# Performance work log

Hardware: AMD Instinct MI355X
Metric: run time of the kernel (lower is better)

The kernel has to match this reference:

```python
import jax, jax.numpy as jnp
import numpy as np

OBJ = 6
N_OBJS = 16
ACT = 32
HID = 128


def _mlp(x, W1, b1, W2, b2, W3, b3):
    # RoboticsMLP with layer_sizes=[128,128]: Linear->ReLU->Linear->ReLU->Linear
    h = jax.nn.relu(x @ W1 + b1)
    h = jax.nn.relu(h @ W2 + b2)
    return h @ W3 + b3


def setup_inputs() -> dict:
    key = jax.random.key(0)
    ks = jax.random.split(key, 16)
    B = 4096
    s = lambda fan_in: 1.0 / np.sqrt(fan_in)
    u_in = OBJ + ACT          # 38
    b_in = 2 * OBJ + ACT      # 44
    return {
        "config": jax.random.normal(ks[0], (B, N_OBJS * OBJ), dtype=jnp.float32),
        "action": jax.random.normal(ks[1], (B, ACT), dtype=jnp.float32),
        "uW1": jax.random.normal(ks[2], (u_in, HID), dtype=jnp.float32) * s(u_in),
        "ub1": jnp.zeros((HID,), jnp.float32),
        "uW2": jax.random.normal(ks[3], (HID, HID), dtype=jnp.float32) * s(HID),
        "ub2": jnp.zeros((HID,), jnp.float32),
        "uW3": jax.random.normal(ks[4], (HID, OBJ), dtype=jnp.float32) * s(HID),
        "ub3": jnp.zeros((OBJ,), jnp.float32),
        "bW1": jax.random.normal(ks[5], (b_in, HID), dtype=jnp.float32) * s(b_in),
        "bb1": jnp.zeros((HID,), jnp.float32),
        "bW2": jax.random.normal(ks[6], (HID, HID), dtype=jnp.float32) * s(HID),
        "bb2": jnp.zeros((HID,), jnp.float32),
        "bW3": jax.random.normal(ks[7], (HID, OBJ), dtype=jnp.float32) * s(HID),
        "bb3": jnp.zeros((OBJ,), jnp.float32),
    }


def reference(config, action, uW1, ub1, uW2, ub2, uW3, ub3,
              bW1, bb1, bW2, bb2, bW3, bb3):
    B = config.shape[0]
    objs = config.reshape(B, N_OBJS, OBJ)                       # [B, N, 6]

    # Unary: per-object MLP on [obj, action]
    act_b = jnp.broadcast_to(action[:, None, :], (B, N_OBJS, ACT))
    u_in = jnp.concatenate([objs, act_b], axis=-1)              # [B, N, 6+A]
    u_out = _mlp(u_in, uW1, ub1, uW2, ub2, uW3, ub3)            # [B, N, 6]

    # Binary: all ordered pairs (i, j), i != j: [obj_i, obj_j, action]
    oi = jnp.broadcast_to(objs[:, :, None, :], (B, N_OBJS, N_OBJS, OBJ))
    oj = jnp.broadcast_to(objs[:, None, :, :], (B, N_OBJS, N_OBJS, OBJ))
    act_p = jnp.broadcast_to(action[:, None, None, :], (B, N_OBJS, N_OBJS, ACT))
    b_in = jnp.concatenate([oi, oj, act_p], axis=-1)            # [B, N, N, 12+A]
    b_out = _mlp(b_in, bW1, bb1, bW2, bb2, bW3, bb3)            # [B, N, N, 6]

    # zero out diagonal (i == j skipped in original) then sum over j
    mask = (1.0 - jnp.eye(N_OBJS, dtype=b_out.dtype))[None, :, :, None]
    b_sum = (b_out * mask).sum(axis=2)                          # [B, N, 6]

    out = objs + u_out + b_sum
    return out.reshape(B, N_OBJS * OBJ)
```

## Files before the change

kernel.cpp:

```cpp
#include <hip/hip_runtime.h>

typedef short bf16x8 __attribute__((ext_vector_type(8)));
typedef float f32x4 __attribute__((ext_vector_type(4)));

__device__ __forceinline__ unsigned short f2bf(float f) {
    unsigned int u = __float_as_uint(f);
    unsigned int r = u + 0x7FFFu + ((u >> 16) & 1u);
    return (unsigned short)(r >> 16);
}

__device__ __forceinline__ unsigned pkbf(float a, float b) {
    unsigned r;
    asm volatile("v_cvt_pk_bf16_f32 %0, %1, %2" : "=v"(r) : "v"(a), "v"(b));
    return r;
}

__global__ __launch_bounds__(256) void prep_all(
        const float* __restrict__ uW1, const float* __restrict__ uW2, const float* __restrict__ uW3,
        const float* __restrict__ bW1, const float* __restrict__ bW2, const float* __restrict__ bW3,
        unsigned short* __restrict__ ws) {
    int idx = blockIdx.x * 256 + threadIdx.x;
    const float* W; int Ksrc, Nsrc, ntsh; unsigned short* dst; int li;
    if (idx < 8192)       { W = uW1; Ksrc = 38;  Nsrc = 128; ntsh = 10; dst = ws;         li = idx; }
    else if (idx < 16384) { W = bW1; Ksrc = 44;  Nsrc = 128; ntsh = 10; dst = ws + 8192;  li = idx - 8192; }
    else if (idx < 32768) { W = uW2; Ksrc = 128; Nsrc = 128; ntsh = 11; dst = ws + 16384; li = idx - 16384; }
    else if (idx < 49152) { W = bW2; Ksrc = 128; Nsrc = 128; ntsh = 11; dst = ws + 32768; li = idx - 32768; }
    else if (idx < 51200) { W = uW3; Ksrc = 128; Nsrc = 6;   ntsh = 11; dst = ws + 49152; li = idx - 49152; }
    else if (idx < 53248) { W = bW3; Ksrc = 128; Nsrc = 6;   ntsh = 11; dst = ws + 51200; li = idx - 51200; }
    else return;
    int e  = li & 7;
    int l  = (li >> 3) & 63;
    int KS = (ntsh == 10) ? 2 : 4;
    int ks = (li >> 9) & (KS - 1);
    int nt = li >> ntsh;
    int k  = ks * 32 + (l >> 4) * 8 + e;
    int n  = nt * 16 + (l & 15);
    float v = (k < Ksrc && n < Nsrc) ? W[k * Nsrc + n] : 0.0f;
    dst[li] = f2bf(v);
}

template <int BINARY>
__global__ __launch_bounds__(256, 3) void mlp_kernel(
        const float* __restrict__ config, const float* __restrict__ action,
        const unsigned short* __restrict__ W1f, const float* __restrict__ b1,
        const unsigned short* __restrict__ W2f, const float* __restrict__ b2,
        const unsigned short* __restrict__ W3f, const float* __restrict__ b3,
        float* __restrict__ out) {
    __shared__ __align__(16) unsigned char smem[4 * 8192];
    const int tid = threadIdx.x;
    const int w = tid >> 6;
    const int l = tid & 63;
    const int g = l >> 4;
    const int c = l & 15;
    unsigned char* buf = smem + w * 8192;

    {
        const int rowL = l >> 1;
        const int kh   = l & 1;
        const int sw   = (rowL & 7) << 4;
        const int base = rowL * 128 + kh * 64;
        const int rg = blockIdx.x * 128 + w * 32 + rowL;
        const int b = rg >> 4;
        const int i = rg & 15;
        const float* cb = config + b * 96;
        const float* ab = action + b * 32;
        if (kh == 0) {
            #pragma unroll
            for (int ch = 0; ch < 4; ++ch) {
                bf16x8 v;
                #pragma unroll
                for (int t8 = 0; t8 < 8; ++t8) {
                    const int k = ch * 8 + t8;
                    float x = (k < 6) ? cb[i * 6 + k] : ab[k - 6];
                    v[t8] = (short)f2bf(x);
                }
                *(bf16x8*)(buf + ((base + ch * 16) ^ sw)) = v;
            }
        } else {
            #pragma unroll
            for (int ch = 0; ch < 4; ++ch) {
                bf16x8 v;
                #pragma unroll
                for (int t8 = 0; t8 < 8; ++t8) {
                    const int k = 32 + ch * 8 + t8;
                    float x = (k < 38) ? ab[k - 6] : 0.0f;
                    v[t8] = (short)f2bf(x);
                }
                *(bf16x8*)(buf + ((base + ch * 16) ^ sw)) = v;
            }
        }
    }
    __syncthreads();

    const f32x4 zero4 = {0.f, 0.f, 0.f, 0.f};

    bf16x8 xf[2][2];
    #pragma unroll
    for (int mt = 0; mt < 2; ++mt)
        #pragma unroll
        for (int ks = 0; ks < 2; ++ks) {
            const int row = mt * 16 + c;
            xf[mt][ks] = *(const bf16x8*)(buf + ((row * 128 + ks * 64 + g * 16) ^ ((c & 7) << 4)));
        }

    #pragma unroll
    for (int nh = 0; nh < 2; ++nh) {
        f32x4 acc[2][4];
        #pragma unroll
        for (int mt = 0; mt < 2; ++mt)
            #pragma unroll
            for (int ntl = 0; ntl < 4; ++ntl) acc[mt][ntl] = zero4;
        #pragma unroll
        for (int ntl = 0; ntl < 4; ++ntl) {
            const int nt = nh * 4 + ntl;
            #pragma unroll
            for (int ks = 0; ks < 2; ++ks) {
                const bf16x8 bfr = *(const bf16x8*)(W1f + ((nt * 2 + ks) * 64 + l) * 8);
                #pragma unroll
                for (int mt = 0; mt < 2; ++mt)
                    acc[mt][ntl] = __builtin_amdgcn_mfma_f32_16x16x32_bf16(xf[mt][ks], bfr, acc[mt][ntl], 0, 0, 0);
            }
        }
        #pragma unroll
        for (int ntl = 0; ntl < 4; ++ntl) {
            const int col = (nh * 4 + ntl) * 16 + c;
            const float bias = b1[col];
            #pragma unroll
            for (int mt = 0; mt < 2; ++mt)
                #pragma unroll
                for (int r = 0; r < 4; ++r) {
                    const int row = mt * 16 + g * 4 + r;
                    const float hv = fmaxf(acc[mt][ntl][r] + bias, 0.f);
                    *(unsigned short*)(buf + ((row * 256 + col * 2) ^ ((row & 7) << 4))) = f2bf(hv);
                }
        }
    }
    __syncthreads();

    bf16x8 hf[2][4];
    #pragma unroll
    for (int mt = 0; mt < 2; ++mt)
        #pragma unroll
        for (int ks = 0; ks < 4; ++ks) {
            const int row = mt * 16 + c;
            hf[mt][ks] = *(const bf16x8*)(buf + ((row * 256 + ks * 64 + g * 16) ^ ((c & 7) << 4)));
        }

    #pragma unroll
    for (int nh = 0; nh < 2; ++nh) {
        f32x4 acc[2][4];
        #pragma unroll
        for (int mt = 0; mt < 2; ++mt)
            #pragma unroll
            for (int ntl = 0; ntl < 4; ++ntl) acc[mt][ntl] = zero4;
        #pragma unroll
        for (int ntl = 0; ntl < 4; ++ntl) {
            const int nt = nh * 4 + ntl;
            #pragma unroll
            for (int ks = 0; ks < 4; ++ks) {
                const bf16x8 bfr = *(const bf16x8*)(W2f + ((nt * 4 + ks) * 64 + l) * 8);
                #pragma unroll
                for (int mt = 0; mt < 2; ++mt)
                    acc[mt][ntl] = __builtin_amdgcn_mfma_f32_16x16x32_bf16(hf[mt][ks], bfr, acc[mt][ntl], 0, 0, 0);
            }
        }
        #pragma unroll
        for (int ntl = 0; ntl < 4; ++ntl) {
            const int col = (nh * 4 + ntl) * 16 + c;
            const float bias = b2[col];
            #pragma unroll
            for (int mt = 0; mt < 2; ++mt)
                #pragma unroll
                for (int r = 0; r < 4; ++r) {
                    const int row = mt * 16 + g * 4 + r;
                    const float hv = fmaxf(acc[mt][ntl][r] + bias, 0.f);
                    *(unsigned short*)(buf + ((row * 256 + col * 2) ^ ((row & 7) << 4))) = f2bf(hv);
                }
        }
    }
    __syncthreads();

    bf16x8 h2f[2][4];
    #pragma unroll
    for (int mt = 0; mt < 2; ++mt)
        #pragma unroll
        for (int ks = 0; ks < 4; ++ks) {
            const int row = mt * 16 + c;
            h2f[mt][ks] = *(const bf16x8*)(buf + ((row * 256 + ks * 64 + g * 16) ^ ((c & 7) << 4)));
        }

    f32x4 acc3[2];
    acc3[0] = zero4; acc3[1] = zero4;
    #pragma unroll
    for (int ks = 0; ks < 4; ++ks) {
        const bf16x8 bfr = *(const bf16x8*)(W3f + (ks * 64 + l) * 8);
        #pragma unroll
        for (int mt = 0; mt < 2; ++mt)
            acc3[mt] = __builtin_amdgcn_mfma_f32_16x16x32_bf16(h2f[mt][ks], bfr, acc3[mt], 0, 0, 0);
    }

    const int rgbase = blockIdx.x * 128 + w * 32;
    const float b3v = (c < 6) ? b3[c] : 0.f;
    #pragma unroll
    for (int mt = 0; mt < 2; ++mt)
        #pragma unroll
        for (int r = 0; r < 4; ++r) {
            const int rg = rgbase + mt * 16 + g * 4 + r;
            const int b = rg >> 4, i = rg & 15;
            if (c < 6) {
                const int idx = b * 96 + i * 6 + c;
                out[idx] = acc3[mt][r] + b3v + config[idx];
            }
        }
}

__global__ __launch_bounds__(256, 3) void binary_kernel(
        const float* __restrict__ config, const float* __restrict__ action,
        const unsigned short* __restrict__ W1f, const float* __restrict__ b1,
        const unsigned short* __restrict__ W2f, const float* __restrict__ b2,
        const unsigned short* __restrict__ W3f, const float* __restrict__ b3,
        float* __restrict__ out) {
    __shared__ __align__(16) unsigned char Ts[4096];
    __shared__ __align__(16) unsigned char PQs[16384];
    __shared__ __align__(16) unsigned char H2s[32768];

    const int tid = threadIdx.x;
    const int w = tid >> 6, l = tid & 63, g = l >> 4, c = l & 15;
    const int b = blockIdx.x >> 1, h = blockIdx.x & 1;
    const float* cb = config + b * 96;
    const float* ab = action + b * 32;
    const f32x4 zero4 = {0.f, 0.f, 0.f, 0.f};

    {
        const int p  = tid >> 3;
        const int k0 = (tid & 7) * 8;
        union { unsigned short us[8]; bf16x8 v; } u;
        #pragma unroll
        for (int e = 0; e < 8; ++e) {
            const int k = k0 + e;
            float x = 0.f;
            if (p < 16) {
                if (k < 6) x = cb[p * 6 + k];
                else if (k >= 12 && k < 44) x = ab[k - 12];
            } else {
                if (k >= 6 && k < 12) x = cb[(p - 16) * 6 + (k - 6)];
            }
            u.us[e] = f2bf(x);
        }
        *(bf16x8*)(Ts + ((p * 128 + k0 * 2) ^ ((p & 7) << 4))) = u.v;
    }
    __syncthreads();

    {
        bf16x8 afr[2][2];
        #pragma unroll
        for (int mt = 0; mt < 2; ++mt)
            #pragma unroll
            for (int ks = 0; ks < 2; ++ks)
                afr[mt][ks] = *(const bf16x8*)(Ts + (((c + 16 * mt) * 128 + 64 * ks + 16 * g) ^ ((c & 7) << 4)));
        f32x4 acc[2][2];
        acc[0][0] = zero4; acc[0][1] = zero4; acc[1][0] = zero4; acc[1][1] = zero4;
        #pragma unroll
        for (int ntl = 0; ntl < 2; ++ntl) {
            const int nt = 2 * w + ntl;
            #pragma unroll
            for (int ks = 0; ks < 2; ++ks) {
                const bf16x8 bfr = *(const bf16x8*)(W1f + ((nt * 2 + ks) * 64 + l) * 8);
                #pragma unroll
                for (int mt = 0; mt < 2; ++mt)
                    acc[mt][ntl] = __builtin_amdgcn_mfma_f32_16x16x32_bf16(afr[mt][ks], bfr, acc[mt][ntl], 0, 0, 0);
            }
        }
        #pragma unroll
        for (int ntl = 0; ntl < 2; ++ntl) {
            const int f = (2 * w + ntl) * 16 + c;
            const float bias = b1[f];
            #pragma unroll
            for (int mt = 0; mt < 2; ++mt)
                #pragma unroll
                for (int r = 0; r < 4; ++r) {
                    const int row = 16 * mt + 4 * g + r;
                    const float v = acc[mt][ntl][r] + (mt == 0 ? bias : 0.f);
                    *(float*)(PQs + ((row * 512 + f * 4) ^ ((row & 7) << 4))) = v;
                }
        }
    }
    __syncthreads();

    const int i0 = h * 8 + 2 * w;
    bf16x8 h1f[2][4];
    #pragma unroll
    for (int nt = 0; nt < 2; ++nt) {
        const int i = i0 + nt;
        #pragma unroll
        for (int ks = 0; ks < 4; ++ks) {
            const int kb = (32 * ks + 8 * g) * 4;
            const f32x4 p0 = *(const f32x4*)(PQs + ((i * 512 + kb) ^ ((i & 7) << 4)));
            const f32x4 p1 = *(const f32x4*)(PQs + ((i * 512 + kb + 16) ^ ((i & 7) << 4)));
            const f32x4 q0 = *(const f32x4*)(PQs + (((16 + c) * 512 + kb) ^ ((c & 7) << 4)));
            const f32x4 q1 = *(const f32x4*)(PQs + (((16 + c) * 512 + kb + 16) ^ ((c & 7) << 4)));
            union { unsigned u[4]; bf16x8 v; } un;
            un.u[0] = pkbf(fmaxf(p0[0] + q0[0], 0.f), fmaxf(p0[1] + q0[1], 0.f));
            un.u[1] = pkbf(fmaxf(p0[2] + q0[2], 0.f), fmaxf(p0[3] + q0[3], 0.f));
            un.u[2] = pkbf(fmaxf(p1[0] + q1[0], 0.f), fmaxf(p1[1] + q1[1], 0.f));
            un.u[3] = pkbf(fmaxf(p1[2] + q1[2], 0.f), fmaxf(p1[3] + q1[3], 0.f));
            h1f[nt][ks] = un.v;
        }
    }

    f32x4 acc2[8][2];
    #pragma unroll
    for (int mt = 0; mt < 8; ++mt) { acc2[mt][0] = zero4; acc2[mt][1] = zero4; }
    #pragma unroll
    for (int mt = 0; mt < 8; ++mt) {
        #pragma unroll
        for (int ks = 0; ks < 4; ++ks) {
            const bf16x8 wf = *(const bf16x8*)(W2f + ((mt * 4 + ks) * 64 + l) * 8);
            acc2[mt][0] = __builtin_amdgcn_mfma_f32_16x16x32_bf16(wf, h1f[0][ks], acc2[mt][0], 0, 0, 0);
            acc2[mt][1] = __builtin_amdgcn_mfma_f32_16x16x32_bf16(wf, h1f[1][ks], acc2[mt][1], 0, 0, 0);
        }
    }

    unsigned char* Hw = H2s + w * 8192;
    #pragma unroll
    for (int mt = 0; mt < 8; ++mt) {
        const f32x4 bv = *(const f32x4*)(b2 + 16 * mt + 4 * g);
        #pragma unroll
        for (int nt = 0; nt < 2; ++nt) {
            const int p = c + 16 * nt;
            uint2 pk2;
            pk2.x = pkbf(fmaxf(acc2[mt][nt][0] + bv[0], 0.f), fmaxf(acc2[mt][nt][1] + bv[1], 0.f));
            pk2.y = pkbf(fmaxf(acc2[mt][nt][2] + bv[2], 0.f), fmaxf(acc2[mt][nt][3] + bv[3], 0.f));
            *(uint2*)(Hw + ((p * 256 + 32 * mt + 8 * g) ^ ((c & 7) << 4))) = pk2;
        }
    }

    f32x4 acc3[2];
    acc3[0] = zero4; acc3[1] = zero4;
    #pragma unroll
    for (int ks = 0; ks < 4; ++ks) {
        const bf16x8 w3 = *(const bf16x8*)(W3f + (ks * 64 + l) * 8);
        #pragma unroll
        for (int mtA = 0; mtA < 2; ++mtA) {
            const bf16x8 hfr = *(const bf16x8*)(Hw + (((c + 16 * mtA) * 256 + 64 * ks + 16 * g) ^ ((c & 7) << 4)));
            acc3[mtA] = __builtin_amdgcn_mfma_f32_16x16x32_bf16(hfr, w3, acc3[mtA], 0, 0, 0);
        }
    }

    const float b3v = (c < 6) ? b3[c] : 0.f;
    #pragma unroll
    for (int mt = 0; mt < 2; ++mt) {
        const int i = i0 + mt;
        float s = 0.f;
        #pragma unroll
        for (int r = 0; r < 4; ++r) {
            const int j = 4 * g + r;
            if (j != i) s += acc3[mt][r] + b3v;
        }
        s += __shfl_xor(s, 16, 64);
        s += __shfl_xor(s, 32, 64);
        if (g == 0 && c < 6) out[b * 96 + i * 6 + c] += s;
    }
}

extern "C" void kernel_launch(void* const* d_in, const int* in_sizes, int n_in,
                              void* d_out, int out_size, void* d_ws, size_t ws_size,
                              hipStream_t stream) {
    const float* config = (const float*)d_in[0];
    const float* action = (const float*)d_in[1];
    const float* uW1 = (const float*)d_in[2];
    const float* ub1 = (const float*)d_in[3];
    const float* uW2 = (const float*)d_in[4];
    const float* ub2 = (const float*)d_in[5];
    const float* uW3 = (const float*)d_in[6];
    const float* ub3 = (const float*)d_in[7];
    const float* bW1 = (const float*)d_in[8];
    const float* bb1 = (const float*)d_in[9];
    const float* bW2 = (const float*)d_in[10];
    const float* bb2 = (const float*)d_in[11];
    const float* bW3 = (const float*)d_in[12];
    const float* bb3 = (const float*)d_in[13];
    float* out = (float*)d_out;

    unsigned short* ws   = (unsigned short*)d_ws;
    unsigned short* uW1f = ws;
    unsigned short* bW1f = ws + 8192;
    unsigned short* uW2f = ws + 16384;
    unsigned short* bW2f = ws + 32768;
    unsigned short* uW3f = ws + 49152;
    unsigned short* bW3f = ws + 51200;

    prep_all<<<208, 256, 0, stream>>>(uW1, uW2, uW3, bW1, bW2, bW3, ws);
    mlp_kernel<0><<<512, 256, 0, stream>>>(config, action, uW1f, ub1, uW2f, ub2, uW3f, ub3, out);
    binary_kernel<<<8192, 256, 0, stream>>>(config, action, bW1f, bb1, bW2f, bb2, bW3f, bb3, out);
}
```

Baseline: 179.8 us.

## Stream layer-2 output chunks into layer-3 MFMA to shrink LDS and raise occupancy

```diff
diff --git a/kernel.cpp b/kernel.cpp
--- a/kernel.cpp
+++ b/kernel.cpp
@@ -39,8 +39,7 @@
     dst[li] = f2bf(v);
 }
 
-template <int BINARY>
-__global__ __launch_bounds__(256, 3) void mlp_kernel(
+__global__ __launch_bounds__(256, 3) void unary_kernel(
         const float* __restrict__ config, const float* __restrict__ action,
         const unsigned short* __restrict__ W1f, const float* __restrict__ b1,
         const unsigned short* __restrict__ W2f, const float* __restrict__ b2,
@@ -62,32 +61,48 @@
         const int rg = blockIdx.x * 128 + w * 32 + rowL;
         const int b = rg >> 4;
         const int i = rg & 15;
-        const float* cb = config + b * 96;
-        const float* ab = action + b * 32;
+        const float* cbr = config + b * 96 + i * 6;
+        const float* ab  = action + b * 32;
         if (kh == 0) {
+            float ov[6];
+            { const float2 t0 = *(const float2*)(cbr);
+              const float2 t1 = *(const float2*)(cbr + 2);
+              const float2 t2 = *(const float2*)(cbr + 4);
+              ov[0]=t0.x; ov[1]=t0.y; ov[2]=t1.x; ov[3]=t1.y; ov[4]=t2.x; ov[5]=t2.y; }
+            float av[26];
+            #pragma unroll
+            for (int q = 0; q < 6; ++q) {
+                const float4 t = *(const float4*)(ab + 4 * q);
+                av[4*q]=t.x; av[4*q+1]=t.y; av[4*q+2]=t.z; av[4*q+3]=t.w;
+            }
+            { const float2 t = *(const float2*)(ab + 24); av[24]=t.x; av[25]=t.y; }
             #pragma unroll
             for (int ch = 0; ch < 4; ++ch) {
-                bf16x8 v;
+                float x[8];
                 #pragma unroll
                 for (int t8 = 0; t8 < 8; ++t8) {
                     const int k = ch * 8 + t8;
-                    float x = (k < 6) ? cb[i * 6 + k] : ab[k - 6];
-                    v[t8] = (short)f2bf(x);
+                    x[t8] = (k < 6) ? ov[k] : av[k - 6];
                 }
-                *(bf16x8*)(buf + ((base + ch * 16) ^ sw)) = v;
+                union { unsigned uu[4]; bf16x8 v; } U;
+                U.uu[0] = pkbf(x[0], x[1]); U.uu[1] = pkbf(x[2], x[3]);
+                U.uu[2] = pkbf(x[4], x[5]); U.uu[3] = pkbf(x[6], x[7]);
+                *(bf16x8*)(buf + ((base + ch * 16) ^ sw)) = U.v;
             }
         } else {
-            #pragma unroll
-            for (int ch = 0; ch < 4; ++ch) {
-                bf16x8 v;
-                #pragma unroll
-                for (int t8 = 0; t8 < 8; ++t8) {
-                    const int k = 32 + ch * 8 + t8;
-                    float x = (k < 38) ? ab[k - 6] : 0.0f;
-                    v[t8] = (short)f2bf(x);
-                }
-                *(bf16x8*)(buf + ((base + ch * 16) ^ sw)) = v;
-            }
+            float av2[6];
+            { const float2 t = *(const float2*)(ab + 26); av2[0]=t.x; av2[1]=t.y; }
+            { const float4 t = *(const float4*)(ab + 28); av2[2]=t.x; av2[3]=t.y; av2[4]=t.z; av2[5]=t.w; }
+            {
+                union { unsigned uu[4]; bf16x8 v; } U;
+                U.uu[0] = pkbf(av2[0], av2[1]); U.uu[1] = pkbf(av2[2], av2[3]);
+                U.uu[2] = pkbf(av2[4], av2[5]); U.uu[3] = 0u;
+                *(bf16x8*)(buf + ((base + 0) ^ sw)) = U.v;
+            }
+            const bf16x8 z = {0,0,0,0,0,0,0,0};
+            *(bf16x8*)(buf + ((base + 16) ^ sw)) = z;
+            *(bf16x8*)(buf + ((base + 32) ^ sw)) = z;
+            *(bf16x8*)(buf + ((base + 48) ^ sw)) = z;
         }
     }
     __syncthreads();
@@ -214,7 +229,7 @@
         }
 }
 
-__global__ __launch_bounds__(256, 3) void binary_kernel(
+__global__ __launch_bounds__(256, 4) void binary_kernel(
         const float* __restrict__ config, const float* __restrict__ action,
         const unsigned short* __restrict__ W1f, const float* __restrict__ b1,
         const unsigned short* __restrict__ W2f, const float* __restrict__ b2,
@@ -222,7 +237,7 @@
         float* __restrict__ out) {
     __shared__ __align__(16) unsigned char Ts[4096];
     __shared__ __align__(16) unsigned char PQs[16384];
-    __shared__ __align__(16) unsigned char H2s[32768];
+    __shared__ __align__(16) unsigned char Cks[8192];
 
     const int tid = threadIdx.x;
     const int w = tid >> 6, l = tid & 63, g = l >> 4, c = l & 15;
@@ -252,37 +267,36 @@
     __syncthreads();
 
     {
-        bf16x8 afr[2][2];
-        #pragma unroll
-        for (int mt = 0; mt < 2; ++mt)
+        bf16x8 tfr[2][2];
+        #pragma unroll
+        for (int nt = 0; nt < 2; ++nt)
             #pragma unroll
             for (int ks = 0; ks < 2; ++ks)
-                afr[mt][ks] = *(const bf16x8*)(Ts + (((c + 16 * mt) * 128 + 64 * ks + 16 * g) ^ ((c & 7) << 4)));
-        f32x4 acc[2][2];
-        acc[0][0] = zero4; acc[0][1] = zero4; acc[1][0] = zero4; acc[1][1] = zero4;
-        #pragma unroll
-        for (int ntl = 0; ntl < 2; ++ntl) {
-            const int nt = 2 * w + ntl;
+                tfr[nt][ks] = *(const bf16x8*)(Ts + (((c + 16 * nt) * 128 + 64 * ks + 16 * g) ^ ((c & 7) << 4)));
+        f32x4 acc1[2][2];
+        acc1[0][0] = zero4; acc1[0][1] = zero4; acc1[1][0] = zero4; acc1[1][1] = zero4;
+        #pragma unroll
+        for (int mt1 = 0; mt1 < 2; ++mt1) {
             #pragma unroll
             for (int ks = 0; ks < 2; ++ks) {
-                const bf16x8 bfr = *(const bf16x8*)(W1f + ((nt * 2 + ks) * 64 + l) * 8);
-                #pragma unroll
-                for (int mt = 0; mt < 2; ++mt)
-                    acc[mt][ntl] = __builtin_amdgcn_mfma_f32_16x16x32_bf16(afr[mt][ks], bfr, acc[mt][ntl], 0, 0, 0);
-            }
-        }
-        #pragma unroll
-        for (int ntl = 0; ntl < 2; ++ntl) {
-            const int f = (2 * w + ntl) * 16 + c;
-            const float bias = b1[f];
-            #pragma unroll
-            for (int mt = 0; mt < 2; ++mt)
-                #pragma unroll
-                for (int r = 0; r < 4; ++r) {
-                    const int row = 16 * mt + 4 * g + r;
-                    const float v = acc[mt][ntl][r] + (mt == 0 ? bias : 0.f);
-                    *(float*)(PQs + ((row * 512 + f * 4) ^ ((row & 7) << 4))) = v;
-                }
+                const bf16x8 wfr = *(const bf16x8*)(W1f + (((2 * w + mt1) * 2 + ks) * 64 + l) * 8);
+                acc1[mt1][0] = __builtin_amdgcn_mfma_f32_16x16x32_bf16(wfr, tfr[0][ks], acc1[mt1][0], 0, 0, 0);
+                acc1[mt1][1] = __builtin_amdgcn_mfma_f32_16x16x32_bf16(wfr, tfr[1][ks], acc1[mt1][1], 0, 0, 0);
+            }
+        }
+        #pragma unroll
+        for (int mt1 = 0; mt1 < 2; ++mt1) {
+            const f32x4 bv = *(const f32x4*)(b1 + 32 * w + 16 * mt1 + 4 * g);
+            acc1[mt1][0] = acc1[mt1][0] + bv;
+            #pragma unroll
+            for (int nt = 0; nt < 2; ++nt) {
+                const int p = c + 16 * nt;
+                const int fb = (32 * w + 16 * mt1 + 4 * g) * 4;
+                float2 v0; v0.x = acc1[mt1][nt][0]; v0.y = acc1[mt1][nt][1];
+                float2 v1; v1.x = acc1[mt1][nt][2]; v1.y = acc1[mt1][nt][3];
+                *(float2*)(PQs + ((p * 512 + fb)     ^ ((p & 7) << 4))) = v0;
+                *(float2*)(PQs + ((p * 512 + fb + 8) ^ ((p & 7) << 4))) = v1;
+            }
         }
     }
     __syncthreads();
@@ -308,54 +322,52 @@
         }
     }
 
-    f32x4 acc2[8][2];
-    #pragma unroll
-    for (int mt = 0; mt < 8; ++mt) { acc2[mt][0] = zero4; acc2[mt][1] = zero4; }
-    #pragma unroll
-    for (int mt = 0; mt < 8; ++mt) {
-        #pragma unroll
-        for (int ks = 0; ks < 4; ++ks) {
-            const bf16x8 wf = *(const bf16x8*)(W2f + ((mt * 4 + ks) * 64 + l) * 8);
-            acc2[mt][0] = __builtin_amdgcn_mfma_f32_16x16x32_bf16(wf, h1f[0][ks], acc2[mt][0], 0, 0, 0);
-            acc2[mt][1] = __builtin_amdgcn_mfma_f32_16x16x32_bf16(wf, h1f[1][ks], acc2[mt][1], 0, 0, 0);
-        }
-    }
-
-    unsigned char* Hw = H2s + w * 8192;
-    #pragma unroll
-    for (int mt = 0; mt < 8; ++mt) {
-        const f32x4 bv = *(const f32x4*)(b2 + 16 * mt + 4 * g);
+    unsigned char* Ck = Cks + w * 2048;
+    f32x4 acc3[2];
+    acc3[0] = zero4; acc3[1] = zero4;
+    #pragma unroll 1
+    for (int ks = 0; ks < 4; ++ks) {
+        f32x4 a2[2][2];
+        a2[0][0] = zero4; a2[0][1] = zero4; a2[1][0] = zero4; a2[1][1] = zero4;
+        #pragma unroll
+        for (int ksp = 0; ksp < 4; ++ksp) {
+            #pragma unroll
+            for (int mt1 = 0; mt1 < 2; ++mt1) {
+                const bf16x8 wf = *(const bf16x8*)(W2f + (((2 * ks + mt1) * 4 + ksp) * 64 + l) * 8);
+                a2[mt1][0] = __builtin_amdgcn_mfma_f32_16x16x32_bf16(wf, h1f[0][ksp], a2[mt1][0], 0, 0, 0);
+                a2[mt1][1] = __builtin_amdgcn_mfma_f32_16x16x32_bf16(wf, h1f[1][ksp], a2[mt1][1], 0, 0, 0);
+            }
+        }
+        #pragma unroll
+        for (int mt1 = 0; mt1 < 2; ++mt1) {
+            const f32x4 bv = *(const f32x4*)(b2 + 32 * ks + 16 * mt1 + 4 * g);
+            #pragma unroll
+            for (int nt = 0; nt < 2; ++nt) {
+                const int p = c + 16 * nt;
+                uint2 pk2;
+                pk2.x = pkbf(fmaxf(a2[mt1][nt][0] + bv[0], 0.f), fmaxf(a2[mt1][nt][1] + bv[1], 0.f));
+                pk2.y = pkbf(fmaxf(a2[mt1][nt][2] + bv[2], 0.f), fmaxf(a2[mt1][nt][3] + bv[3], 0.f));
+                *(uint2*)(Ck + ((p * 64 + 32 * mt1 + 8 * g) ^ (((p >> 1) & 3) << 4))) = pk2;
+            }
+        }
+        const bf16x8 w3 = *(const bf16x8*)(W3f + (ks * 64 + l) * 8);
         #pragma unroll
         for (int nt = 0; nt < 2; ++nt) {
             const int p = c + 16 * nt;
-            uint2 pk2;
-            pk2.x = pkbf(fmaxf(acc2[mt][nt][0] + bv[0], 0.f), fmaxf(acc2[mt][nt][1] + bv[1], 0.f));
-            pk2.y = pkbf(fmaxf(acc2[mt][nt][2] + bv[2], 0.f), fmaxf(acc2[mt][nt][3] + bv[3], 0.f));
-            *(uint2*)(Hw + ((p * 256 + 32 * mt + 8 * g) ^ ((c & 7) << 4))) = pk2;
-        }
-    }
-
-    f32x4 acc3[2];
-    acc3[0] = zero4; acc3[1] = zero4;
-    #pragma unroll
-    for (int ks = 0; ks < 4; ++ks) {
-        const bf16x8 w3 = *(const bf16x8*)(W3f + (ks * 64 + l) * 8);
-        #pragma unroll
-        for (int mtA = 0; mtA < 2; ++mtA) {
-            const bf16x8 hfr = *(const bf16x8*)(Hw + (((c + 16 * mtA) * 256 + 64 * ks + 16 * g) ^ ((c & 7) << 4)));
-            acc3[mtA] = __builtin_amdgcn_mfma_f32_16x16x32_bf16(hfr, w3, acc3[mtA], 0, 0, 0);
+            const bf16x8 ha = *(const bf16x8*)(Ck + ((p * 64 + 16 * g) ^ (((p >> 1) & 3) << 4)));
+            acc3[nt] = __builtin_amdgcn_mfma_f32_16x16x32_bf16(ha, w3, acc3[nt], 0, 0, 0);
         }
     }
 
     const float b3v = (c < 6) ? b3[c] : 0.f;
     #pragma unroll
-    for (int mt = 0; mt < 2; ++mt) {
-        const int i = i0 + mt;
+    for (int nt = 0; nt < 2; ++nt) {
+        const int i = i0 + nt;
         float s = 0.f;
         #pragma unroll
         for (int r = 0; r < 4; ++r) {
             const int j = 4 * g + r;
-            if (j != i) s += acc3[mt][r] + b3v;
+            if (j != i) s += acc3[nt][r] + b3v;
         }
         s += __shfl_xor(s, 16, 64);
         s += __shfl_xor(s, 32, 64);
@@ -391,6 +403,6 @@
     unsigned short* bW3f = ws + 51200;
 
     prep_all<<<208, 256, 0, stream>>>(uW1, uW2, uW3, bW1, bW2, bW3, ws);
-    mlp_kernel<0><<<512, 256, 0, stream>>>(config, action, uW1f, ub1, uW2f, ub2, uW3f, ub3, out);
+    unary_kernel<<<512, 256, 0, stream>>>(config, action, uW1f, ub1, uW2f, ub2, uW3f, ub3, out);
     binary_kernel<<<8192, 256, 0, stream>>>(config, action, bW1f, bb1, bW2f, bb2, bW3f, bb3, out);
 }
```

Result: faster. 163.8 us (-8.9%).
